# Optimization experiments

Measured on AMD Instinct MI355X. Metric: run time of the kernel, lower is better.

The kernel has to match this reference:

```python
import jax, jax.numpy as jnp
import numpy as np

N = 100000
E = 1600000
DIM_NODE = 128
DIM_HIDDEN = 64
NUM_CLASSES = 10
BN_EPS = 1e-5


def gcn_conv(h_in, W, b, src, dst, num_nodes):
    # h_in: [N, d_in], W: [d_out, d_in] (torch Linear layout), b: [d_out]
    h = h_in @ W.T  # [N, d_out]
    # add self-loops with weight 1 (PyG gcn_norm default, add_self_loops=True)
    loop = jnp.arange(num_nodes, dtype=src.dtype)
    row = jnp.concatenate([src, loop])
    col = jnp.concatenate([dst, loop])
    ew = jnp.ones(row.shape[0], dtype=h.dtype)
    # symmetric degree normalization: deg over target nodes
    deg = jax.ops.segment_sum(ew, col, num_segments=num_nodes)
    dinv = jnp.where(deg > 0, jax.lax.rsqrt(deg), 0.0)
    norm = dinv[row] * ew * dinv[col]  # [E+N]
    msg = h[row] * norm[:, None]  # gather + scale, [E+N, d_out]
    out = jax.ops.segment_sum(msg, col, num_segments=num_nodes)  # scatter-add
    return out + b


def batchnorm_gelu(h, gamma, beta):
    # training-mode BatchNorm1d over node dim, then exact GELU
    mean = jnp.mean(h, axis=0)
    var = jnp.var(h, axis=0)  # biased, as torch BN uses for normalization
    hn = (h - mean) * jax.lax.rsqrt(var + BN_EPS) * gamma + beta
    return jax.nn.gelu(hn, approximate=False)


def setup_inputs() -> dict:
    key = jax.random.key(0)
    ks = jax.random.split(key, 20)
    x = jax.random.normal(ks[0], (N, DIM_NODE), dtype=jnp.float32)
    edge_index = jax.random.randint(ks[1], (2, E), 0, N, dtype=jnp.int32)

    def lin(k, dout, din):
        s = 1.0 / np.sqrt(din)
        kw, kb = jax.random.split(k)
        W = jax.random.uniform(kw, (dout, din), minval=-s, maxval=s, dtype=jnp.float32)
        b = jax.random.uniform(kb, (dout,), minval=-s, maxval=s, dtype=jnp.float32)
        return W, b

    W1, b1 = lin(ks[2], DIM_HIDDEN, DIM_NODE)
    W2, b2 = lin(ks[3], DIM_HIDDEN, DIM_HIDDEN)
    W3, b3 = lin(ks[4], DIM_HIDDEN, DIM_HIDDEN)
    Wf, bf = lin(ks[5], NUM_CLASSES, DIM_HIDDEN)
    g1 = jnp.ones((DIM_HIDDEN,), jnp.float32); be1 = jnp.zeros((DIM_HIDDEN,), jnp.float32)
    g2 = jnp.ones((DIM_HIDDEN,), jnp.float32); be2 = jnp.zeros((DIM_HIDDEN,), jnp.float32)
    g3 = jnp.ones((DIM_HIDDEN,), jnp.float32); be3 = jnp.zeros((DIM_HIDDEN,), jnp.float32)
    return {"x": x, "edge_index": edge_index,
            "W1": W1, "b1": b1, "g1": g1, "be1": be1,
            "W2": W2, "b2": b2, "g2": g2, "be2": be2,
            "W3": W3, "b3": b3, "g3": g3, "be3": be3,
            "Wf": Wf, "bf": bf}


def reference(x, edge_index, W1, b1, g1, be1, W2, b2, g2, be2, W3, b3, g3, be3, Wf, bf):
    src, dst = edge_index[0], edge_index[1]
    h = batchnorm_gelu(gcn_conv(x, W1, b1, src, dst, N), g1, be1)
    h = batchnorm_gelu(gcn_conv(h, W2, b2, src, dst, N), g2, be2)
    h = batchnorm_gelu(gcn_conv(h, W3, b3, src, dst, N), g3, be3)
    # ffn: Dropout (identity in eval) + Linear; second forward def returns logits (no softmax)
    return h @ Wf.T + bf
```

## Files before the change

kernel.cpp:

```cpp
#include <hip/hip_runtime.h>
#include <hip/hip_fp16.h>
#include <math.h>

#define N_NODES 100000
#define N_EDGES 1600000
#define D_IN    128
#define D_H     64
#define N_CLS   10
#define BN_EPS  1e-5f

#define RANGES  8
#define RSIZE   12500
#define CAP2    16
#define ZROW    N_NODES
#define GBLK    1024
#define TILES   3125
#define GEMM0_B 6250

typedef _Float16 f16x8 __attribute__((ext_vector_type(8)));
typedef float f32x4 __attribute__((ext_vector_type(4)));

__device__ __forceinline__ float gelu_exact(float x) {
    return 0.5f * x * (1.0f + erff(x * 0.70710678118654752f));
}

__device__ __forceinline__ f16x8 to_h8(float4 a, float4 b) {
    f16x8 h;
    h[0] = (_Float16)a.x; h[1] = (_Float16)a.y;
    h[2] = (_Float16)a.z; h[3] = (_Float16)a.w;
    h[4] = (_Float16)b.x; h[5] = (_Float16)b.y;
    h[6] = (_Float16)b.z; h[7] = (_Float16)b.w;
    return h;
}

__device__ __forceinline__ void acc8s(float* a, uint4 p, float d) {
    float2 f0 = __half22float2(*(const __half2*)&p.x);
    float2 f1 = __half22float2(*(const __half2*)&p.y);
    float2 f2 = __half22float2(*(const __half2*)&p.z);
    float2 f3 = __half22float2(*(const __half2*)&p.w);
    a[0] = fmaf(d, f0.x, a[0]); a[1] = fmaf(d, f0.y, a[1]);
    a[2] = fmaf(d, f1.x, a[2]); a[3] = fmaf(d, f1.y, a[3]);
    a[4] = fmaf(d, f2.x, a[4]); a[5] = fmaf(d, f2.y, a[5]);
    a[6] = fmaf(d, f3.x, a[6]); a[7] = fmaf(d, f3.y, a[7]);
}

__global__ __launch_bounds__(256) void k_build(const int* __restrict__ src,
                                               const int* __restrict__ dst,
                                               int* __restrict__ cnt2,
                                               unsigned short* __restrict__ slot2,
                                               const float* __restrict__ x,
                                               const float* __restrict__ W1,
                                               __half* __restrict__ out) {
    const int t = threadIdx.x;

    if (blockIdx.x & 1) {
        int e = (blockIdx.x >> 1) * 256 + t;
        if (e < N_EDGES) {
            int d = dst[e];
            int s = src[e];
            unsigned r = (unsigned)s / (unsigned)RSIZE;
            int pos = atomicAdd(&cnt2[r * N_NODES + d], 1);
            if (pos < CAP2)
                slot2[(size_t)(r * CAP2 + pos) * N_NODES + d] =
                    (unsigned short)(s - (int)r * RSIZE);
        }
        return;
    }

    const int tile = blockIdx.x >> 1;
    const int base = tile * 16;

    if (tile == 0 && t < 16) {
        ((uint2*)(out + (size_t)ZROW * 64))[t] = make_uint2(0u, 0u);
    }

    const int l = t & 63;
    const int w = t >> 6;
    const int row16 = l & 15;
    const int kg = l >> 4;
    const int node = base + row16;
    const int f = w * 16 + row16;

    f16x8 afr[4], bfr[4];
#pragma unroll
    for (int s = 0; s < 4; ++s) {
        const int kb = s * 32 + kg * 8;
        const float4* wp = (const float4*)&W1[f * D_IN + kb];
        bfr[s] = to_h8(wp[0], wp[1]);
        const float4* xp = (const float4*)&x[(size_t)node * D_IN + kb];
        afr[s] = to_h8(xp[0], xp[1]);
    }
    f32x4 c = {0.f, 0.f, 0.f, 0.f};
#pragma unroll
    for (int s = 0; s < 4; ++s)
        c = __builtin_amdgcn_mfma_f32_16x16x32_f16(afr[s], bfr[s], c, 0, 0, 0);

#pragma unroll
    for (int r = 0; r < 4; ++r)
        out[(size_t)(base + kg * 4 + r) * 64 + f] = __float2half(c[r]);
}

__global__ void k_prep(const int* __restrict__ cnt2, float* __restrict__ dinv, int n) {
    int i = blockIdx.x * blockDim.x + threadIdx.x;
    if (i < n) {
        int deg = 0;
#pragma unroll
        for (int r = 0; r < RANGES; ++r) deg += cnt2[r * N_NODES + i];
        dinv[i] = rsqrtf((float)(deg + 1));
    }
    if (i == 0) dinv[ZROW] = 0.f;
}

__global__ __launch_bounds__(256) void k_gemm64(const __half* __restrict__ in,
                                                const float* __restrict__ W,
                                                const float* __restrict__ colsum,
                                                const float* __restrict__ gamma,
                                                const float* __restrict__ beta,
                                                __half* __restrict__ out) {
    __shared__ float sscale[64], sshift[64];
    __shared__ _Float16 sact[16][72];
    const int t = threadIdx.x;
    const int base = blockIdx.x * 16;

    if (t < 64) {
        float mean = colsum[t] * (1.0f / N_NODES);
        float var = colsum[64 + t] * (1.0f / N_NODES) - mean * mean;
        float sc = gamma[t] * rsqrtf(var + BN_EPS);
        sscale[t] = sc;
        sshift[t] = beta[t] - mean * sc;
    }
    __syncthreads();

    {
        const int n = t >> 4, k0 = (t & 15) * 4;
        const __half2* p = (const __half2*)(in + (size_t)(base + n) * 64 + k0);
        float2 f0 = __half22float2(p[0]);
        float2 f1 = __half22float2(p[1]);
        float4 sc = *(const float4*)&sscale[k0];
        float4 sh = *(const float4*)&sshift[k0];
        sact[n][k0 + 0] = (_Float16)gelu_exact(f0.x * sc.x + sh.x);
        sact[n][k0 + 1] = (_Float16)gelu_exact(f0.y * sc.y + sh.y);
        sact[n][k0 + 2] = (_Float16)gelu_exact(f1.x * sc.z + sh.z);
        sact[n][k0 + 3] = (_Float16)gelu_exact(f1.y * sc.w + sh.w);
    }
    __syncthreads();

    const int l = t & 63;
    const int w = t >> 6;
    const int row16 = l & 15;
    const int kg = l >> 4;
    const int f = w * 16 + row16;

    f16x8 bfr[2];
#pragma unroll
    for (int s = 0; s < 2; ++s) {
        const int kb = s * 32 + kg * 8;
        const float4* wp = (const float4*)&W[f * D_H + kb];
        bfr[s] = to_h8(wp[0], wp[1]);
    }
    f32x4 c = {0.f, 0.f, 0.f, 0.f};
#pragma unroll
    for (int s = 0; s < 2; ++s) {
        f16x8 a = *(const f16x8*)&sact[row16][s * 32 + kg * 8];
        c = __builtin_amdgcn_mfma_f32_16x16x32_f16(a, bfr[s], c, 0, 0, 0);
    }
#pragma unroll
    for (int r = 0; r < 4; ++r)
        out[(size_t)(base + kg * 4 + r) * 64 + f] = __float2half(c[r]);
}

__global__ __launch_bounds__(256, 4) void k_gather(const int* __restrict__ cnt2,
                                                   const unsigned short* __restrict__ slot2,
                                                   const __half* __restrict__ hs,
                                                   const float* __restrict__ dinv,
                                                   const float* __restrict__ bias,
                                                   __half* __restrict__ y,
                                                   float* __restrict__ colsum) {
    __shared__ float rs[4][64];
    __shared__ float rss[4][64];

    const int t = threadIdx.x;
    const int lane = t & 63;
    const int w = t >> 6;
    const int q = lane & 7;
    const int s = lane >> 3;
    const int xcd = blockIdx.x & 7;

    int tiles[4];
    int ntile = 0;
    for (int g = blockIdx.x; g < TILES; g += GBLK) tiles[ntile++] = g;

    float acc[4][8];
#pragma unroll
    for (int ti = 0; ti < 4; ++ti)
#pragma unroll
        for (int r = 0; r < 8; ++r) acc[ti][r] = 0.f;

#pragma unroll
    for (int ti = 0; ti < 4; ++ti) {
        if (ti < ntile) {
            int v = tiles[ti] * 32 + w * 8 + s;
            acc8s(acc[ti], *(const uint4*)&hs[(size_t)v * 64 + q * 8], dinv[v]);
        }
    }

    for (int k = 0; k < RANGES; ++k) {
        const int r = (xcd + k) & 7;
        const int rbase = r * RSIZE;
        const size_t slab = (size_t)r * CAP2 * N_NODES;
#pragma unroll
        for (int ti = 0; ti < 4; ++ti) {
            if (ti >= ntile) continue;
            const int v = tiles[ti] * 32 + w * 8 + s;
            const int deg = min(cnt2[r * N_NODES + v], CAP2);
            int md = deg;
#pragma unroll
            for (int m = 8; m <= 32; m <<= 1) md = max(md, __shfl_xor(md, m));

            for (int j = 0; j < md; j += 4) {
                uint4 p[4];
                float du[4];
#pragma unroll
                for (int b = 0; b < 4; ++b) {
                    int idx = j + b;
                    int sv = slot2[slab + (size_t)idx * N_NODES + v];
                    int u = (idx < deg) ? (rbase + sv) : ZROW;
                    du[b] = dinv[u];
                    p[b] = *(const uint4*)&hs[(size_t)u * 64 + q * 8];
                }
#pragma unroll
                for (int b = 0; b < 4; ++b) acc8s(acc[ti], p[b], du[b]);
            }
        }
    }

    float sum[8], sq[8];
#pragma unroll
    for (int r = 0; r < 8; ++r) { sum[r] = 0.f; sq[r] = 0.f; }

#pragma unroll
    for (int ti = 0; ti < 4; ++ti) {
        if (ti >= ntile) continue;
        const int v = tiles[ti] * 32 + w * 8 + s;
        const float d = dinv[v];
        float yv[8];
#pragma unroll
        for (int r = 0; r < 8; ++r) {
            yv[r] = d * acc[ti][r] + bias[q * 8 + r];
            sum[r] += yv[r];
            sq[r] += yv[r] * yv[r];
        }
        uint4 pk;
        __half2* ph = (__half2*)&pk;
        ph[0] = __floats2half2_rn(yv[0], yv[1]);
        ph[1] = __floats2half2_rn(yv[2], yv[3]);
        ph[2] = __floats2half2_rn(yv[4], yv[5]);
        ph[3] = __floats2half2_rn(yv[6], yv[7]);
        *(uint4*)&y[(size_t)v * 64 + q * 8] = pk;
    }

#pragma unroll
    for (int m = 8; m <= 32; m <<= 1) {
#pragma unroll
        for (int r = 0; r < 8; ++r) {
            sum[r] += __shfl_xor(sum[r], m);
            sq[r] += __shfl_xor(sq[r], m);
        }
    }
    if (s == 0) {
#pragma unroll
        for (int r = 0; r < 8; ++r) {
            rs[w][q * 8 + r] = sum[r];
            rss[w][q * 8 + r] = sq[r];
        }
    }
    __syncthreads();
    if (t < 64) {
        atomicAdd(&colsum[t], rs[0][t] + rs[1][t] + rs[2][t] + rs[3][t]);
        atomicAdd(&colsum[64 + t], rss[0][t] + rss[1][t] + rss[2][t] + rss[3][t]);
    }
}

__global__ __launch_bounds__(256) void k_out(const __half* __restrict__ h,
                                             const float* __restrict__ Wf,
                                             const float* __restrict__ bf,
                                             const float* __restrict__ colsum,
                                             const float* __restrict__ gamma,
                                             const float* __restrict__ beta,
                                             float* __restrict__ out, int n) {
    __shared__ float sh[64 * 65];
    __shared__ float sW[N_CLS * 65];
    __shared__ float sb[N_CLS];
    __shared__ float sscale[64], sshift[64];
    const int t = threadIdx.x;
    const int base = blockIdx.x * 64;

    if (t < 64) {
        float mean = colsum[t] * (1.0f / N_NODES);
        float var = colsum[64 + t] * (1.0f / N_NODES) - mean * mean;
        float sc = gamma[t] * rsqrtf(var + BN_EPS);
        sscale[t] = sc;
        sshift[t] = beta[t] - mean * sc;
    }
    __syncthreads();

    const uint4* h8 = (const uint4*)(h + (size_t)base * 64);
    for (int i = t; i < 64 * 64 / 8; i += 256) {
        uint4 p = h8[i];
        int vv = i >> 3, k = (i & 7) * 8;
        float2 f0 = __half22float2(*(const __half2*)&p.x);
        float2 f1 = __half22float2(*(const __half2*)&p.y);
        float2 f2 = __half22float2(*(const __half2*)&p.z);
        float2 f3 = __half22float2(*(const __half2*)&p.w);
        sh[vv * 65 + k + 0] = gelu_exact(f0.x * sscale[k + 0] + sshift[k + 0]);
        sh[vv * 65 + k + 1] = gelu_exact(f0.y * sscale[k + 1] + sshift[k + 1]);
        sh[vv * 65 + k + 2] = gelu_exact(f1.x * sscale[k + 2] + sshift[k + 2]);
        sh[vv * 65 + k + 3] = gelu_exact(f1.y * sscale[k + 3] + sshift[k + 3]);
        sh[vv * 65 + k + 4] = gelu_exact(f2.x * sscale[k + 4] + sshift[k + 4]);
        sh[vv * 65 + k + 5] = gelu_exact(f2.y * sscale[k + 5] + sshift[k + 5]);
        sh[vv * 65 + k + 6] = gelu_exact(f3.x * sscale[k + 6] + sshift[k + 6]);
        sh[vv * 65 + k + 7] = gelu_exact(f3.y * sscale[k + 7] + sshift[k + 7]);
    }
    for (int i = t; i < N_CLS * 64; i += 256) {
        int c = i / 64, k = i % 64;
        sW[c * 65 + k] = Wf[i];
    }
    if (t < N_CLS) sb[t] = bf[t];
    __syncthreads();
    for (int o = t; o < 64 * N_CLS; o += 256) {
        int v = o / N_CLS, c = o % N_CLS;
        if (base + v < n) {
            float a = sb[c];
#pragma unroll
            for (int k = 0; k < 64; ++k) a += sh[v * 65 + k] * sW[c * 65 + k];
            out[(base + v) * N_CLS + c] = a;
        }
    }
}

extern "C" void kernel_launch(void* const* d_in, const int* in_sizes, int n_in,
                              void* d_out, int out_size, void* d_ws, size_t ws_size,
                              hipStream_t stream) {
    const float* x   = (const float*)d_in[0];
    const int*   ei  = (const int*)d_in[1];
    const float* W1  = (const float*)d_in[2];
    const float* b1  = (const float*)d_in[3];
    const float* g1  = (const float*)d_in[4];
    const float* be1 = (const float*)d_in[5];
    const float* W2  = (const float*)d_in[6];
    const float* b2  = (const float*)d_in[7];
    const float* g2  = (const float*)d_in[8];
    const float* be2 = (const float*)d_in[9];
    const float* W3  = (const float*)d_in[10];
    const float* b3  = (const float*)d_in[11];
    const float* g3  = (const float*)d_in[12];
    const float* be3 = (const float*)d_in[13];
    const float* Wf  = (const float*)d_in[14];
    const float* bfc = (const float*)d_in[15];

    const int* src = ei;
    const int* dst = ei + N_EDGES;

    char*   w0      = (char*)d_ws;
    __half* A       = (__half*)w0;
    __half* B       = A + ((size_t)N_NODES + 1) * 64;
    float*  dinv    = (float*)(B + (size_t)N_NODES * 64);
    int*    cnt2    = (int*)(dinv + N_NODES + 1);
    float*  colsum2 = (float*)(cnt2 + RANGES * N_NODES);
    unsigned short* slot2 = (unsigned short*)(colsum2 + 3 * 128);

    hipMemsetAsync(cnt2, 0, RANGES * N_NODES * sizeof(int) + 3 * 128 * sizeof(float),
                   stream);

    k_build<<<2 * GEMM0_B, 256, 0, stream>>>(src, dst, cnt2, slot2, x, W1, A);
    k_prep<<<(N_NODES + 255) / 256, 256, 0, stream>>>(cnt2, dinv, N_NODES);

    k_gather<<<GBLK, 256, 0, stream>>>(cnt2, slot2, A, dinv, b1, B, colsum2);
    k_gemm64<<<GEMM0_B, 256, 0, stream>>>(B, W2, colsum2, g1, be1, A);
    k_gather<<<GBLK, 256, 0, stream>>>(cnt2, slot2, A, dinv, b2, B, colsum2 + 128);
    k_gemm64<<<GEMM0_B, 256, 0, stream>>>(B, W3, colsum2 + 128, g2, be2, A);
    k_gather<<<GBLK, 256, 0, stream>>>(cnt2, slot2, A, dinv, b3, B, colsum2 + 256);
    k_out<<<(N_NODES + 63) / 64, 256, 0, stream>>>(B, Wf, bfc, colsum2 + 256, g3, be3,
                                                   (float*)d_out, N_NODES);
}
```

Before: 526.1 us.

## Pre-scale source features by dinv to drop per-edge dinv gathers

```diff
diff --git a/kernel.cpp b/kernel.cpp
--- a/kernel.cpp
+++ b/kernel.cpp
@@ -16,6 +16,7 @@
 #define GBLK    1024
 #define TILES   3125
 #define GEMM0_B 6250
+#define FILL_B  1563
 
 typedef _Float16 f16x8 __attribute__((ext_vector_type(8)));
 typedef float f32x4 __attribute__((ext_vector_type(4)));
@@ -33,15 +34,15 @@
     return h;
 }
 
-__device__ __forceinline__ void acc8s(float* a, uint4 p, float d) {
+__device__ __forceinline__ void acc8(float* a, uint4 p) {
     float2 f0 = __half22float2(*(const __half2*)&p.x);
     float2 f1 = __half22float2(*(const __half2*)&p.y);
     float2 f2 = __half22float2(*(const __half2*)&p.z);
     float2 f3 = __half22float2(*(const __half2*)&p.w);
-    a[0] = fmaf(d, f0.x, a[0]); a[1] = fmaf(d, f0.y, a[1]);
-    a[2] = fmaf(d, f1.x, a[2]); a[3] = fmaf(d, f1.y, a[3]);
-    a[4] = fmaf(d, f2.x, a[4]); a[5] = fmaf(d, f2.y, a[5]);
-    a[6] = fmaf(d, f3.x, a[6]); a[7] = fmaf(d, f3.y, a[7]);
+    a[0] += f0.x; a[1] += f0.y;
+    a[2] += f1.x; a[3] += f1.y;
+    a[4] += f2.x; a[5] += f2.y;
+    a[6] += f3.x; a[7] += f3.y;
 }
 
 __global__ __launch_bounds__(256) void k_build(const int* __restrict__ src,
@@ -53,21 +54,34 @@
                                                __half* __restrict__ out) {
     const int t = threadIdx.x;
 
-    if (blockIdx.x & 1) {
-        int e = (blockIdx.x >> 1) * 256 + t;
-        if (e < N_EDGES) {
-            int d = dst[e];
-            int s = src[e];
-            unsigned r = (unsigned)s / (unsigned)RSIZE;
-            int pos = atomicAdd(&cnt2[r * N_NODES + d], 1);
-            if (pos < CAP2)
-                slot2[(size_t)(r * CAP2 + pos) * N_NODES + d] =
-                    (unsigned short)(s - (int)r * RSIZE);
+    if (blockIdx.x < FILL_B) {
+        const int e0 = blockIdx.x * 1024 + t;
+        int d4[4], s4[4];
+        bool ok[4];
+#pragma unroll
+        for (int i = 0; i < 4; ++i) {
+            int e = e0 + i * 256;
+            ok[i] = (e < N_EDGES);
+            d4[i] = ok[i] ? dst[e] : 0;
+            s4[i] = ok[i] ? src[e] : 0;
+        }
+        unsigned r4[4];
+        int pos4[4];
+#pragma unroll
+        for (int i = 0; i < 4; ++i) {
+            r4[i] = (unsigned)s4[i] / (unsigned)RSIZE;
+            pos4[i] = ok[i] ? atomicAdd(&cnt2[r4[i] * N_NODES + d4[i]], 1) : CAP2;
+        }
+#pragma unroll
+        for (int i = 0; i < 4; ++i) {
+            if (pos4[i] < CAP2)
+                slot2[(size_t)(r4[i] * CAP2 + pos4[i]) * N_NODES + d4[i]] =
+                    (unsigned short)(s4[i] - (int)r4[i] * RSIZE);
         }
         return;
     }
 
-    const int tile = blockIdx.x >> 1;
+    const int tile = blockIdx.x - FILL_B;
     const int base = tile * 16;
 
     if (tile == 0 && t < 16) {
@@ -100,15 +114,28 @@
         out[(size_t)(base + kg * 4 + r) * 64 + f] = __float2half(c[r]);
 }
 
-__global__ void k_prep(const int* __restrict__ cnt2, float* __restrict__ dinv, int n) {
-    int i = blockIdx.x * blockDim.x + threadIdx.x;
-    if (i < n) {
-        int deg = 0;
-#pragma unroll
-        for (int r = 0; r < RANGES; ++r) deg += cnt2[r * N_NODES + i];
-        dinv[i] = rsqrtf((float)(deg + 1));
-    }
-    if (i == 0) dinv[ZROW] = 0.f;
+__global__ __launch_bounds__(256) void k_prep(const int* __restrict__ cnt2,
+                                              float* __restrict__ dinv,
+                                              __half* __restrict__ hs) {
+    const int t = threadIdx.x;
+    const int node = blockIdx.x * 32 + (t >> 3);
+    const int seg = t & 7;
+    int deg = 0;
+#pragma unroll
+    for (int r = 0; r < RANGES; ++r) deg += cnt2[r * N_NODES + node];
+    float di = rsqrtf((float)(deg + 1));
+    if (seg == 0) dinv[node] = di;
+    if (blockIdx.x == 0 && t == 0) dinv[ZROW] = 0.f;
+
+    uint4* row = (uint4*)(hs + (size_t)node * 64);
+    uint4 p = row[seg];
+    __half2* ph = (__half2*)&p;
+#pragma unroll
+    for (int i = 0; i < 4; ++i) {
+        float2 f = __half22float2(ph[i]);
+        ph[i] = __floats2half2_rn(f.x * di, f.y * di);
+    }
+    row[seg] = p;
 }
 
 __global__ __launch_bounds__(256) void k_gemm64(const __half* __restrict__ in,
@@ -116,6 +143,7 @@
                                                 const float* __restrict__ colsum,
                                                 const float* __restrict__ gamma,
                                                 const float* __restrict__ beta,
+                                                const float* __restrict__ dinv,
                                                 __half* __restrict__ out) {
     __shared__ float sscale[64], sshift[64];
     __shared__ _Float16 sact[16][72];
@@ -165,8 +193,10 @@
         c = __builtin_amdgcn_mfma_f32_16x16x32_f16(a, bfr[s], c, 0, 0, 0);
     }
 #pragma unroll
-    for (int r = 0; r < 4; ++r)
-        out[(size_t)(base + kg * 4 + r) * 64 + f] = __float2half(c[r]);
+    for (int r = 0; r < 4; ++r) {
+        const int node = base + kg * 4 + r;
+        out[(size_t)node * 64 + f] = __float2half(dinv[node] * c[r]);
+    }
 }
 
 __global__ __launch_bounds__(256, 4) void k_gather(const int* __restrict__ cnt2,
@@ -200,7 +230,7 @@
     for (int ti = 0; ti < 4; ++ti) {
         if (ti < ntile) {
             int v = tiles[ti] * 32 + w * 8 + s;
-            acc8s(acc[ti], *(const uint4*)&hs[(size_t)v * 64 + q * 8], dinv[v]);
+            acc8(acc[ti], *(const uint4*)&hs[(size_t)v * 64 + q * 8]);
         }
     }
 
@@ -219,17 +249,15 @@
 
             for (int j = 0; j < md; j += 4) {
                 uint4 p[4];
-                float du[4];
 #pragma unroll
                 for (int b = 0; b < 4; ++b) {
                     int idx = j + b;
                     int sv = slot2[slab + (size_t)idx * N_NODES + v];
                     int u = (idx < deg) ? (rbase + sv) : ZROW;
-                    du[b] = dinv[u];
                     p[b] = *(const uint4*)&hs[(size_t)u * 64 + q * 8];
                 }
 #pragma unroll
-                for (int b = 0; b < 4; ++b) acc8s(acc[ti], p[b], du[b]);
+                for (int b = 0; b < 4; ++b) acc8(acc[ti], p[b]);
             }
         }
     }
@@ -372,13 +400,13 @@
     hipMemsetAsync(cnt2, 0, RANGES * N_NODES * sizeof(int) + 3 * 128 * sizeof(float),
                    stream);
 
-    k_build<<<2 * GEMM0_B, 256, 0, stream>>>(src, dst, cnt2, slot2, x, W1, A);
-    k_prep<<<(N_NODES + 255) / 256, 256, 0, stream>>>(cnt2, dinv, N_NODES);
+    k_build<<<FILL_B + GEMM0_B, 256, 0, stream>>>(src, dst, cnt2, slot2, x, W1, A);
+    k_prep<<<TILES, 256, 0, stream>>>(cnt2, dinv, A);
 
     k_gather<<<GBLK, 256, 0, stream>>>(cnt2, slot2, A, dinv, b1, B, colsum2);
-    k_gemm64<<<GEMM0_B, 256, 0, stream>>>(B, W2, colsum2, g1, be1, A);
+    k_gemm64<<<GEMM0_B, 256, 0, stream>>>(B, W2, colsum2, g1, be1, dinv, A);
     k_gather<<<GBLK, 256, 0, stream>>>(cnt2, slot2, A, dinv, b2, B, colsum2 + 128);
-    k_gemm64<<<GEMM0_B, 256, 0, stream>>>(B, W3, colsum2 + 128, g2, be2, A);
+    k_gemm64<<<GEMM0_B, 256, 0, stream>>>(B, W3, colsum2 + 128, g2, be2, dinv, A);
     k_gather<<<GBLK, 256, 0, stream>>>(cnt2, slot2, A, dinv, b3, B, colsum2 + 256);
     k_out<<<(N_NODES + 63) / 64, 256, 0, stream>>>(B, Wf, bfc, colsum2 + 256, g3, be3,
                                                    (float*)d_out, N_NODES);
```

After: 574.4 us. 9.2% more time.
